# Kernel tuning notes

Measured on AMD Instinct MI355X. Metric: run time of the kernel, lower is better.

Reference implementation:

```python
import jax, jax.numpy as jnp
import numpy as np

N_HEADS = 16

def setup_inputs() -> dict:
    key = jax.random.key(0)
    k1, k2, k3, k4 = jax.random.split(key, 4)
    B, N, E = 4, 2048, 1024
    x = jax.random.normal(k1, (B, N, E), dtype=jnp.float32)
    s = 1.0 / np.sqrt(E)
    Wq = jax.random.normal(k2, (E, E), dtype=jnp.float32) * s
    Wk = jax.random.normal(k3, (E, E), dtype=jnp.float32) * s
    Wv = jax.random.normal(k4, (E, E), dtype=jnp.float32) * s
    return {"x": x, "Wq": Wq, "Wk": Wk, "Wv": Wv}

def reference(x, Wq, Wk, Wv):
    # first_block=False -> PositionalEncoding is identity: encoded_vectors = x
    B, N, E = x.shape
    H = N_HEADS
    D = E // H
    norm = np.sqrt(D).astype(np.float32)
    # torch nn.Linear(bias=False): y = x @ W.T
    q = (x @ Wq.T).reshape(B, N, H, D).transpose(0, 2, 1, 3)  # [B,H,N,D]
    k = (x @ Wk.T).reshape(B, N, H, D).transpose(0, 2, 1, 3)
    v = (x @ Wv.T).reshape(B, N, H, D).transpose(0, 2, 1, 3)
    scores = jnp.einsum('bhnd,bhmd->bhnm', q, k) / norm  # [B,H,N,N]
    attn = jax.nn.softmax(scores, axis=-1)
    # original einsum 'stuu, stuv -> stuv': diagonal of attn scales values
    diag = jnp.diagonal(attn, axis1=-2, axis2=-1)  # [B,H,N]
    av = diag[..., None] * v  # [B,H,N,D]
    av = av.transpose(0, 2, 1, 3).reshape(B, N, E)
    return (av, x)
```

## Files before the change

### kernel.cpp

```cpp
#include <hip/hip_runtime.h>
#include <hip/hip_bf16.h>
#include <stdint.h>

typedef __attribute__((ext_vector_type(8))) short short8;
typedef __attribute__((ext_vector_type(4))) float f32x4;

#define BATCH 4
#define SEQ   2048
#define EMB   1024
#define HEADS 16
#define DHEAD 64
#define MROWS (BATCH * SEQ)

#define QSCALE 0.18033688011112042f

__device__ inline unsigned short f2bf(float f) {
    unsigned int u = __float_as_uint(f);
    unsigned int r = (u + 0x7fffu + ((u >> 16) & 1u)) >> 16;
    return (unsigned short)r;
}

__device__ __forceinline__ void gl_lds16(const short* g, short* l) {
    __builtin_amdgcn_global_load_lds(
        (const __attribute__((address_space(1))) void*)g,
        (__attribute__((address_space(3))) void*)l, 16, 0, 0);
}

template <int N>
__device__ __forceinline__ void waitvm() {
    asm volatile("s_waitcnt vmcnt(%0)" :: "n"(N) : "memory");
}

__global__ __launch_bounds__(256) void pack_x(const float* __restrict__ src,
                                              unsigned short* __restrict__ dst,
                                              float* __restrict__ pass) {
    int i = (blockIdx.x * 256 + threadIdx.x) * 8;
    const float4* s = reinterpret_cast<const float4*>(src + i);
    float4 f0 = s[0];
    float4 f1 = s[1];
    union { unsigned short u[8]; short8 v; } o;
    o.u[0] = f2bf(f0.x); o.u[1] = f2bf(f0.y); o.u[2] = f2bf(f0.z); o.u[3] = f2bf(f0.w);
    o.u[4] = f2bf(f1.x); o.u[5] = f2bf(f1.y); o.u[6] = f2bf(f1.z); o.u[7] = f2bf(f1.w);
    *reinterpret_cast<short8*>(dst + i) = o.v;
    float4* p = reinterpret_cast<float4*>(pass + i);
    p[0] = f0;
    p[1] = f1;
}

__global__ __launch_bounds__(256) void pack_w3(const float* __restrict__ wq,
                                               const float* __restrict__ wk,
                                               const float* __restrict__ wv,
                                               unsigned short* __restrict__ dq,
                                               unsigned short* __restrict__ dk,
                                               unsigned short* __restrict__ dv) {
    const float* src = blockIdx.y == 0 ? wq : blockIdx.y == 1 ? wk : wv;
    unsigned short* dst = blockIdx.y == 0 ? dq : blockIdx.y == 1 ? dk : dv;
    int i = (blockIdx.x * 256 + threadIdx.x) * 8;
    const float4* s = reinterpret_cast<const float4*>(src + i);
    float4 f0 = s[0];
    float4 f1 = s[1];
    union { unsigned short u[8]; short8 v; } o;
    o.u[0] = f2bf(f0.x); o.u[1] = f2bf(f0.y); o.u[2] = f2bf(f0.z); o.u[3] = f2bf(f0.w);
    o.u[4] = f2bf(f1.x); o.u[5] = f2bf(f1.y); o.u[6] = f2bf(f1.z); o.u[7] = f2bf(f1.w);
    *reinterpret_cast<short8*>(dst + i) = o.v;
}

template <int MODE>
__global__ __launch_bounds__(512, 2) void gemm8(const short* __restrict__ A,
                                                const short* __restrict__ Bm,
                                                unsigned short* __restrict__ Cb,
                                                float* __restrict__ out,
                                                const float* __restrict__ dgp) {
    constexpr int K = EMB;
    constexpr int NT = K / 32;
    constexpr int BN = (MODE == 0) ? 256 : 128;
    constexpr int NF = BN / 64;
    constexpr int BUFSTRIDE = 8192 + BN * 32;
    constexpr int VW = 2 + BN / 128;

    __shared__ short Ks[3 * BUFSTRIDE];

    const int t = threadIdx.x;
    const int lane = t & 63;
    const int w = t >> 6;
    const int wr = w >> 2;
    const int wc = w & 3;
    const int rl = lane & 15;
    const int pg = (lane >> 4) ^ (lane & 3);
    const int m0 = blockIdx.x * 256;
    const int n0 = blockIdx.y * BN;

    const int sr = t >> 2;
    const int sg = (t & 3) ^ (sr & 3);
    const int soff = sr * K + sg * 8;
    const short* gA0 = A + (size_t)(m0)*K + soff;
    const short* gA1 = A + (size_t)(m0 + 128) * K + soff;
    const short* gB0 = Bm + (size_t)(n0)*K + soff;
    const short* gB1 = Bm + (size_t)(n0 + 128) * K + soff;
    short* ldsw = Ks + w * 512;

#define STAGE8(kk, bb)                                               \
    {                                                                \
        const int _k = (kk)*32;                                      \
        short* _l = ldsw + (bb)*BUFSTRIDE;                           \
        gl_lds16(gA0 + _k, _l);                                      \
        gl_lds16(gA1 + _k, _l + 4096);                               \
        gl_lds16(gB0 + _k, _l + 8192);                               \
        if (MODE == 0) gl_lds16(gB1 + _k, _l + 12288);               \
    }

    f32x4 acc[8][NF] = {};

    STAGE8(0, 0);
    STAGE8(1, 1);
    waitvm<VW>();
    __builtin_amdgcn_s_barrier();

    int cur = 0;
    for (int kt = 0; kt < NT; ++kt) {
        const int pf = kt + 2;
        if (pf < NT) {
            int nb = cur + 2; if (nb >= 3) nb -= 3;
            STAGE8(pf, nb);
        }

        const short* bufp = Ks + cur * BUFSTRIDE;
        short8 av[8], bv[NF];
#pragma unroll
        for (int i = 0; i < 8; i++)
            av[i] = *(const short8*)&bufp[wr * 4096 + i * 512 + rl * 32 + pg * 8];
#pragma unroll
        for (int j = 0; j < NF; j++) {
            const int brow = (MODE == 0) ? ((wc & 1) * 64 + j * 16 + rl)
                                         : (wc * 32 + j * 16 + rl);
            const int bh = (MODE == 0) ? (wc >> 1) : 0;
            bv[j] = *(const short8*)&bufp[8192 + bh * 4096 + brow * 32 + pg * 8];
        }

        __builtin_amdgcn_s_setprio(1);
#pragma unroll
        for (int i = 0; i < 8; i++)
#pragma unroll
            for (int j = 0; j < NF; j++)
                acc[i][j] = __builtin_amdgcn_mfma_f32_16x16x32_bf16(av[i], bv[j], acc[i][j], 0, 0, 0);
        __builtin_amdgcn_s_setprio(0);

        if (kt < NT - 2) waitvm<VW>();
        else             waitvm<0>();
        __builtin_amdgcn_s_barrier();

        cur += 1; if (cur == 3) cur = 0;
    }
#undef STAGE8

    const int gr_base = m0 + wr * 128 + (lane >> 4) * 4;
    const int gc_base = n0 + wc * (BN / 4) + rl;
#pragma unroll
    for (int i = 0; i < 8; i++) {
#pragma unroll
        for (int j = 0; j < NF; j++) {
            const int col = gc_base + j * 16;
#pragma unroll
            for (int r = 0; r < 4; r++) {
                const int grow = gr_base + i * 16 + r;
                const int bb = grow >> 11;
                const int nn = grow & 2047;
                if (MODE == 0) {
                    const int sel = col >> 10;
                    const int cc = col & 1023;
                    const int hh = cc >> 6;
                    const int dd = cc & 63;
                    const float sc = sel ? 1.0f : QSCALE;
                    Cb[(((size_t)((sel << 6) + (bb << 4) + hh) * SEQ + nn) << 6) + dd] =
                        f2bf(acc[i][j][r] * sc);
                } else {
                    const int hh = col >> 6;
                    const float d = dgp[((bb << 4) + hh) * SEQ + nn];
                    out[(size_t)grow * EMB + col] = acc[i][j][r] * d;
                }
            }
        }
    }
}

#define KT 128

__global__ __launch_bounds__(512, 4) void diag_kernel(const short* __restrict__ Qh,
                                                      const short* __restrict__ Kh,
                                                      float* __restrict__ dgp) {
    const int n = blockIdx.x;
    const int bh = (n & 7) | ((n >> 6) << 3);
    const int qt = (n >> 3) & 7;
    __shared__ short Ksd[2][KT][64];

    const int t = threadIdx.x;
    const int lane = t & 63;
    const int w = t >> 6;
    const int rl = lane & 15;
    const int g = lane >> 4;
    const int kq = g * 8;

    const short* Kbh = Kh + (size_t)bh * SEQ * DHEAD;
    const short* Qbh = Qh + (size_t)bh * SEQ * DHEAD;

    const int qbase = qt * 256 + w * 32;
    short8 a0[2], a1[2];
#pragma unroll
    for (int i = 0; i < 2; i++) {
        const int qrow = qbase + i * 16 + rl;
        a0[i] = *(const short8*)(Qbh + qrow * DHEAD + kq);
        a1[i] = *(const short8*)(Qbh + qrow * DHEAD + kq + 32);
    }

    float sdiag[2];
    const int rr = rl - g * 4;
#pragma unroll
    for (int i = 0; i < 2; i++) {
        const int krow = qbase + i * 16 + rl;
        const short8 b0d = *(const short8*)(Kbh + krow * DHEAD + kq);
        const short8 b1d = *(const short8*)(Kbh + krow * DHEAD + kq + 32);
        f32x4 cd = {};
        cd = __builtin_amdgcn_mfma_f32_16x16x32_bf16(a0[i], b0d, cd, 0, 0, 0);
        cd = __builtin_amdgcn_mfma_f32_16x16x32_bf16(a1[i], b1d, cd, 0, 0, 0);
        sdiag[i] = (rr >= 0 && rr < 4) ? cd[rr] : 0.f;
    }

    const int r0 = t >> 3;
    const int c0 = t & 7;
    const int cs = (c0 ^ (r0 & 7)) * 8;

    *(short8*)&Ksd[0][r0][cs]      = *(const short8*)&Kbh[r0 * DHEAD + c0 * 8];
    *(short8*)&Ksd[0][r0 + 64][cs] = *(const short8*)&Kbh[(r0 + 64) * DHEAD + c0 * 8];
    __syncthreads();

    const int blk0 = (g ^ (lane & 7)) * 8;
    const int blk1 = ((g + 4) ^ (lane & 7)) * 8;

    float ssum[2][4] = {};
    int buf = 0;

    for (int kt = 0; kt < SEQ / KT; ++kt) {
        short8 p0, p1;
        if (kt < SEQ / KT - 1) {
            const short* src = Kbh + (kt + 1) * KT * DHEAD;
            p0 = *(const short8*)&src[r0 * DHEAD + c0 * 8];
            p1 = *(const short8*)&src[(r0 + 64) * DHEAD + c0 * 8];
        }
#pragma unroll
        for (int sub = 0; sub < 8; ++sub) {
            const int row = sub * 16 + rl;
            const short8 b0 = *(const short8*)&Ksd[buf][row][blk0];
            const short8 b1 = *(const short8*)&Ksd[buf][row][blk1];
            f32x4 c[2];
#pragma unroll
            for (int i = 0; i < 2; i++) {
                c[i] = __builtin_amdgcn_mfma_f32_16x16x32_bf16(a0[i], b0, f32x4{}, 0, 0, 0);
                c[i] = __builtin_amdgcn_mfma_f32_16x16x32_bf16(a1[i], b1, c[i], 0, 0, 0);
            }
#pragma unroll
            for (int i = 0; i < 2; i++)
#pragma unroll
                for (int r = 0; r < 4; ++r)
                    ssum[i][r] += __builtin_amdgcn_exp2f(c[i][r]);
        }
        if (kt < SEQ / KT - 1) {
            __syncthreads();
            *(short8*)&Ksd[buf ^ 1][r0][cs]      = p0;
            *(short8*)&Ksd[buf ^ 1][r0 + 64][cs] = p1;
            __syncthreads();
        }
        buf ^= 1;
    }

#pragma unroll
    for (int i = 0; i < 2; i++)
#pragma unroll
        for (int r = 0; r < 4; r++) {
            float v = ssum[i][r];
            v += __shfl_xor(v, 1);
            v += __shfl_xor(v, 2);
            v += __shfl_xor(v, 4);
            v += __shfl_xor(v, 8);
            ssum[i][r] = v;
        }

    if (rr >= 0 && rr < 4) {
#pragma unroll
        for (int i = 0; i < 2; i++) {
            const float dg = __builtin_amdgcn_exp2f(sdiag[i]) / ssum[i][rr];
            dgp[bh * SEQ + qbase + i * 16 + rl] = dg;
        }
    }
}

extern "C" void kernel_launch(void* const* d_in, const int* in_sizes, int n_in,
                              void* d_out, int out_size, void* d_ws, size_t ws_size,
                              hipStream_t stream) {
    const float* x  = (const float*)d_in[0];
    const float* Wq = (const float*)d_in[1];
    const float* Wk = (const float*)d_in[2];
    const float* Wv = (const float*)d_in[3];
    float* out = (float*)d_out;
    char* ws = (char*)d_ws;

    const size_t xb_off  = 0;
    const size_t wq_off  = xb_off + (size_t)MROWS * EMB * 2;
    const size_t wk_off  = wq_off + (size_t)EMB * EMB * 2;
    const size_t wv_off  = wk_off + (size_t)EMB * EMB * 2;
    const size_t q_off   = wv_off + (size_t)EMB * EMB * 2;
    const size_t k_off   = q_off + (size_t)MROWS * EMB * 2;
    const size_t dg_off  = k_off + (size_t)MROWS * EMB * 2;

    short* xb  = (short*)(ws + xb_off);
    short* wqb = (short*)(ws + wq_off);
    short* wkb = (short*)(ws + wk_off);
    short* wvb = (short*)(ws + wv_off);
    short* Qh  = (short*)(ws + q_off);
    short* Kh  = (short*)(ws + k_off);
    float* dgp = (float*)(ws + dg_off);

    const int nx = MROWS * EMB;
    const int nw = EMB * EMB;

    pack_x<<<nx / 2048, 256, 0, stream>>>(x, (unsigned short*)xb,
                                          out + (size_t)MROWS * EMB);
    pack_w3<<<dim3(nw / 2048, 3), 256, 0, stream>>>(Wq, Wk, Wv,
                                                    (unsigned short*)wqb,
                                                    (unsigned short*)wkb,
                                                    (unsigned short*)wvb);

    gemm8<0><<<dim3(MROWS / 256, 2048 / 256), 512, 0, stream>>>(
        xb, wqb, (unsigned short*)Qh, nullptr, nullptr);

    diag_kernel<<<BATCH * HEADS * (SEQ / 256), 512, 0, stream>>>(Qh, Kh, dgp);

    gemm8<1><<<dim3(MROWS / 256, EMB / 128), 512, 0, stream>>>(
        xb, wvb, nullptr, out, dgp);
}
```

Baseline: 129.3 us.

## Triple-buffer K tiles via direct global-to-LDS loads in diag kernel; merge pack kernels

The diag kernel now streams K tiles straight from global memory into a three-slot LDS ring using global_load_lds, prefetching two tiles ahead. It replaces the register-staged double buffer that needed two barriers per tile with a single vmcnt wait and one barrier. The MFMA and exp2 accumulation steps are interleaved across two alternating accumulator sets to hide latency. Separately, the x and weight pack kernels are merged into one launch to save a kernel launch. The LDS footprint grows from two tiles to three, which may lower occupancy.

```diff
diff --git a/kernel.cpp b/kernel.cpp
--- a/kernel.cpp
+++ b/kernel.cpp
@@ -11,6 +11,7 @@
 #define HEADS 16
 #define DHEAD 64
 #define MROWS (BATCH * SEQ)
+#define NW    (EMB * EMB)
 
 #define QSCALE 0.18033688011112042f
 
@@ -31,38 +32,37 @@
     asm volatile("s_waitcnt vmcnt(%0)" :: "n"(N) : "memory");
 }
 
-__global__ __launch_bounds__(256) void pack_x(const float* __restrict__ src,
-                                              unsigned short* __restrict__ dst,
-                                              float* __restrict__ pass) {
-    int i = (blockIdx.x * 256 + threadIdx.x) * 8;
-    const float4* s = reinterpret_cast<const float4*>(src + i);
+__global__ __launch_bounds__(256) void pack_all(const float* __restrict__ x,
+                                                const float* __restrict__ wq,
+                                                const float* __restrict__ wk,
+                                                const float* __restrict__ wv,
+                                                unsigned short* __restrict__ xb,
+                                                unsigned short* __restrict__ wb,
+                                                float* __restrict__ pass) {
+    const int i = (blockIdx.x * 256 + threadIdx.x) * 8;
+    const float* src;
+    unsigned short* dst;
+    bool isx = i < MROWS * EMB;
+    if (isx) {
+        src = x + i;
+        dst = xb + i;
+    } else {
+        const int j = i - MROWS * EMB;
+        src = (j < NW) ? wq + j : (j < 2 * NW) ? wk + (j - NW) : wv + (j - 2 * NW);
+        dst = wb + j;
+    }
+    const float4* s = reinterpret_cast<const float4*>(src);
     float4 f0 = s[0];
     float4 f1 = s[1];
     union { unsigned short u[8]; short8 v; } o;
     o.u[0] = f2bf(f0.x); o.u[1] = f2bf(f0.y); o.u[2] = f2bf(f0.z); o.u[3] = f2bf(f0.w);
     o.u[4] = f2bf(f1.x); o.u[5] = f2bf(f1.y); o.u[6] = f2bf(f1.z); o.u[7] = f2bf(f1.w);
-    *reinterpret_cast<short8*>(dst + i) = o.v;
-    float4* p = reinterpret_cast<float4*>(pass + i);
-    p[0] = f0;
-    p[1] = f1;
-}
-
-__global__ __launch_bounds__(256) void pack_w3(const float* __restrict__ wq,
-                                               const float* __restrict__ wk,
-                                               const float* __restrict__ wv,
-                                               unsigned short* __restrict__ dq,
-                                               unsigned short* __restrict__ dk,
-                                               unsigned short* __restrict__ dv) {
-    const float* src = blockIdx.y == 0 ? wq : blockIdx.y == 1 ? wk : wv;
-    unsigned short* dst = blockIdx.y == 0 ? dq : blockIdx.y == 1 ? dk : dv;
-    int i = (blockIdx.x * 256 + threadIdx.x) * 8;
-    const float4* s = reinterpret_cast<const float4*>(src + i);
-    float4 f0 = s[0];
-    float4 f1 = s[1];
-    union { unsigned short u[8]; short8 v; } o;
-    o.u[0] = f2bf(f0.x); o.u[1] = f2bf(f0.y); o.u[2] = f2bf(f0.z); o.u[3] = f2bf(f0.w);
-    o.u[4] = f2bf(f1.x); o.u[5] = f2bf(f1.y); o.u[6] = f2bf(f1.z); o.u[7] = f2bf(f1.w);
-    *reinterpret_cast<short8*>(dst + i) = o.v;
+    *reinterpret_cast<short8*>(dst) = o.v;
+    if (isx) {
+        float4* p = reinterpret_cast<float4*>(pass + i);
+        p[0] = f0;
+        p[1] = f1;
+    }
 }
 
 template <int MODE>
@@ -183,7 +183,7 @@
     }
 }
 
-#define KT 128
+#define DNT (SEQ / 128)
 
 __global__ __launch_bounds__(512, 4) void diag_kernel(const short* __restrict__ Qh,
                                                       const short* __restrict__ Kh,
@@ -191,7 +191,7 @@
     const int n = blockIdx.x;
     const int bh = (n & 7) | ((n >> 6) << 3);
     const int qt = (n >> 3) & 7;
-    __shared__ short Ksd[2][KT][64];
+    __shared__ short Ksd[3 * 8192];
 
     const int t = threadIdx.x;
     const int lane = t & 63;
@@ -225,52 +225,81 @@
         sdiag[i] = (rr >= 0 && rr < 4) ? cd[rr] : 0.f;
     }
 
-    const int r0 = t >> 3;
-    const int c0 = t & 7;
-    const int cs = (c0 ^ (r0 & 7)) * 8;
-
-    *(short8*)&Ksd[0][r0][cs]      = *(const short8*)&Kbh[r0 * DHEAD + c0 * 8];
-    *(short8*)&Ksd[0][r0 + 64][cs] = *(const short8*)&Kbh[(r0 + 64) * DHEAD + c0 * 8];
-    __syncthreads();
+    const int sr = t >> 3;
+    const int sb = ((t & 7) ^ (sr & 7)) * 8;
+    const short* gK0 = Kbh + sr * DHEAD + sb;
+    const short* gK1 = Kbh + (sr + 64) * DHEAD + sb;
+    short* ldsw = Ksd + w * 512;
+
+#define DSTAGE(kk, bb)                                    \
+    {                                                     \
+        gl_lds16(gK0 + (kk)*8192, ldsw + (bb)*8192);      \
+        gl_lds16(gK1 + (kk)*8192, ldsw + (bb)*8192 + 4096); \
+    }
 
     const int blk0 = (g ^ (lane & 7)) * 8;
     const int blk1 = ((g + 4) ^ (lane & 7)) * 8;
 
     float ssum[2][4] = {};
-    int buf = 0;
-
-    for (int kt = 0; kt < SEQ / KT; ++kt) {
-        short8 p0, p1;
-        if (kt < SEQ / KT - 1) {
-            const short* src = Kbh + (kt + 1) * KT * DHEAD;
-            p0 = *(const short8*)&src[r0 * DHEAD + c0 * 8];
-            p1 = *(const short8*)&src[(r0 + 64) * DHEAD + c0 * 8];
-        }
-#pragma unroll
-        for (int sub = 0; sub < 8; ++sub) {
-            const int row = sub * 16 + rl;
-            const short8 b0 = *(const short8*)&Ksd[buf][row][blk0];
-            const short8 b1 = *(const short8*)&Ksd[buf][row][blk1];
-            f32x4 c[2];
-#pragma unroll
-            for (int i = 0; i < 2; i++) {
-                c[i] = __builtin_amdgcn_mfma_f32_16x16x32_bf16(a0[i], b0, f32x4{}, 0, 0, 0);
-                c[i] = __builtin_amdgcn_mfma_f32_16x16x32_bf16(a1[i], b1, c[i], 0, 0, 0);
-            }
-#pragma unroll
-            for (int i = 0; i < 2; i++)
-#pragma unroll
-                for (int r = 0; r < 4; ++r)
-                    ssum[i][r] += __builtin_amdgcn_exp2f(c[i][r]);
-        }
-        if (kt < SEQ / KT - 1) {
-            __syncthreads();
-            *(short8*)&Ksd[buf ^ 1][r0][cs]      = p0;
-            *(short8*)&Ksd[buf ^ 1][r0 + 64][cs] = p1;
-            __syncthreads();
-        }
-        buf ^= 1;
-    }
+
+    DSTAGE(0, 0);
+    DSTAGE(1, 1);
+    waitvm<2>();
+    __builtin_amdgcn_s_barrier();
+
+#define QKMFMA(sub, c)                                                          \
+    {                                                                           \
+        const short* _r = bufp + ((sub)*16 + rl) * 64;                          \
+        const short8 _b0 = *(const short8*)(_r + blk0);                         \
+        const short8 _b1 = *(const short8*)(_r + blk1);                         \
+        c[0] = __builtin_amdgcn_mfma_f32_16x16x32_bf16(a0[0], _b0, f32x4{}, 0, 0, 0); \
+        c[0] = __builtin_amdgcn_mfma_f32_16x16x32_bf16(a1[0], _b1, c[0], 0, 0, 0);    \
+        c[1] = __builtin_amdgcn_mfma_f32_16x16x32_bf16(a0[1], _b0, f32x4{}, 0, 0, 0); \
+        c[1] = __builtin_amdgcn_mfma_f32_16x16x32_bf16(a1[1], _b1, c[1], 0, 0, 0);    \
+    }
+#define EXPACC(c)                                         \
+    {                                                     \
+        _Pragma("unroll") for (int i = 0; i < 2; i++)     \
+        _Pragma("unroll") for (int r = 0; r < 4; ++r)     \
+            ssum[i][r] += __builtin_amdgcn_exp2f(c[i][r]); \
+    }
+
+    int cur = 0;
+    for (int kt = 0; kt < DNT; ++kt) {
+        if (kt + 2 < DNT) {
+            int nb = cur + 2; if (nb >= 3) nb -= 3;
+            DSTAGE(kt + 2, nb);
+        }
+        const short* bufp = Ksd + cur * 8192;
+
+        f32x4 cE[2], cO[2];
+        QKMFMA(0, cE);
+        QKMFMA(1, cO);
+        EXPACC(cE);
+        QKMFMA(2, cE);
+        EXPACC(cO);
+        QKMFMA(3, cO);
+        EXPACC(cE);
+        QKMFMA(4, cE);
+        EXPACC(cO);
+        QKMFMA(5, cO);
+        EXPACC(cE);
+        QKMFMA(6, cE);
+        EXPACC(cO);
+        QKMFMA(7, cO);
+        EXPACC(cE);
+        EXPACC(cO);
+
+        if (kt < DNT - 1) {
+            if (kt < DNT - 2) waitvm<2>();
+            else              waitvm<0>();
+            __builtin_amdgcn_s_barrier();
+        }
+        cur += 1; if (cur == 3) cur = 0;
+    }
+#undef DSTAGE
+#undef QKMFMA
+#undef EXPACC
 
 #pragma unroll
     for (int i = 0; i < 2; i++)
@@ -305,29 +334,24 @@
 
     const size_t xb_off  = 0;
     const size_t wq_off  = xb_off + (size_t)MROWS * EMB * 2;
-    const size_t wk_off  = wq_off + (size_t)EMB * EMB * 2;
-    const size_t wv_off  = wk_off + (size_t)EMB * EMB * 2;
-    const size_t q_off   = wv_off + (size_t)EMB * EMB * 2;
+    const size_t wk_off  = wq_off + (size_t)NW * 2;
+    const size_t wv_off  = wk_off + (size_t)NW * 2;
+    const size_t q_off   = wv_off + (size_t)NW * 2;
     const size_t k_off   = q_off + (size_t)MROWS * EMB * 2;
     const size_t dg_off  = k_off + (size_t)MROWS * EMB * 2;
 
     short* xb  = (short*)(ws + xb_off);
     short* wqb = (short*)(ws + wq_off);
-    short* wkb = (short*)(ws + wk_off);
     short* wvb = (short*)(ws + wv_off);
     short* Qh  = (short*)(ws + q_off);
     short* Kh  = (short*)(ws + k_off);
     float* dgp = (float*)(ws + dg_off);
 
-    const int nx = MROWS * EMB;
-    const int nw = EMB * EMB;
-
-    pack_x<<<nx / 2048, 256, 0, stream>>>(x, (unsigned short*)xb,
-                                          out + (size_t)MROWS * EMB);
-    pack_w3<<<dim3(nw / 2048, 3), 256, 0, stream>>>(Wq, Wk, Wv,
-                                                    (unsigned short*)wqb,
-                                                    (unsigned short*)wkb,
-                                                    (unsigned short*)wvb);
+    const int npack = (MROWS * EMB + 3 * NW) / 2048;
+
+    pack_all<<<npack, 256, 0, stream>>>(x, Wq, Wk, Wv,
+                                        (unsigned short*)xb, (unsigned short*)wqb,
+                                        out + (size_t)MROWS * EMB);
 
     gemm8<0><<<dim3(MROWS / 256, 2048 / 256), 512, 0, stream>>>(
         xb, wqb, (unsigned short*)Qh, nullptr, nullptr);
```

New measurement: 128.9 us. No clear change (-0.3%).
